# Kernel tuning notes

Hardware: AMD Instinct MI355X
Metric: run time of the kernel (lower is better)

The kernel has to match this reference:

```python
import jax, jax.numpy as jnp
import numpy as np

B, S, D = 4, 8192, 512


def setup_inputs() -> dict:
    key = jax.random.key(0)
    k1, k2, k3 = jax.random.split(key, 3)
    input_real = jax.random.normal(k1, (B, S, D), dtype=jnp.float32)
    input_imag = jax.random.normal(k2, (B, S, D), dtype=jnp.float32)
    weight = jax.random.uniform(k3, (B, S), dtype=jnp.float32)
    return {"input_real": input_real, "input_imag": input_imag, "weight": weight}


def reference(input_real, input_imag, weight):
    # Original: sum_s w[b,s] * (r_s r_s^T + i_s i_s^T)  and  sum_s w[b,s] * (i_s r_s^T - r_s i_s^T).
    # Algebraically equal to weighted Gram GEMMs X^T diag(w) Y; avoids the [B,S,D,D] intermediate.
    def wgram(x, y):
        # [B,S,D] x [B,S] x [B,S,D] -> [B,D,D]
        return jnp.einsum('bsd,bs,bse->bde', x, weight, y)

    output_r = wgram(input_real, input_real) + wgram(input_imag, input_imag)
    output_i = wgram(input_imag, input_real) - wgram(input_real, input_imag)
    return (output_r, output_i)
```

## Files before the change

### kernel.cpp

```cpp
#include <hip/hip_runtime.h>
#include <cstdint>
#include <cstddef>

#define NB 4
#define NS 8192
#define ND 512
#define NP 1024
#define BK 32

typedef __bf16 bf16x8 __attribute__((ext_vector_type(8)));
typedef float f32x4 __attribute__((ext_vector_type(4)));

union FragU { uint4 u; bf16x8 h; };

__device__ __forceinline__ unsigned short bf16rne(float x) {
  unsigned int u = __builtin_bit_cast(unsigned int, x);
  u += 0x7FFFu + ((u >> 16) & 1u);
  return (unsigned short)(u >> 16);
}

__device__ __forceinline__ void gload16(const void* g, void* l) {
  __builtin_amdgcn_global_load_lds(
      (const __attribute__((address_space(1))) unsigned int*)g,
      (__attribute__((address_space(3))) unsigned int*)l, 16, 0, 0);
}

__global__ __launch_bounds__(256)
void k_prep(const float* __restrict__ R, const float* __restrict__ I,
            const float* __restrict__ W, unsigned short* __restrict__ Yt) {
  __shared__ unsigned short L[64][66];
  const int t   = threadIdx.x;
  const int blk = blockIdx.x;
  const int sb  = blk & 127;
  const int pb  = (blk >> 7) & 15;
  const int b   = blk >> 11;
  const float* src = (pb < 8) ? R : I;
  const int col0 = (pb & 7) * 64;
  const int s0 = sb * 64;
  const int dl = (t & 15) * 4;
  const int sl0 = t >> 4;
#pragma unroll
  for (int r = 0; r < 4; ++r) {
    const int sl = sl0 + r * 16;
    const int s  = s0 + sl;
    const float sw = sqrtf(W[b * NS + s]);
    const float4 v = *(const float4*)(src + (size_t)(b * NS + s) * ND + col0 + dl);
    L[sl][dl + 0] = bf16rne(v.x * sw);
    L[sl][dl + 1] = bf16rne(v.y * sw);
    L[sl][dl + 2] = bf16rne(v.z * sw);
    L[sl][dl + 3] = bf16rne(v.w * sw);
  }
  __syncthreads();
  const int pl0 = t >> 3;
  const int sc  = (t & 7) * 8;
#pragma unroll
  for (int r = 0; r < 2; ++r) {
    const int pl = pl0 + r * 32;
    uint4 o;
    o.x = (unsigned)L[sc + 0][pl] | ((unsigned)L[sc + 1][pl] << 16);
    o.y = (unsigned)L[sc + 2][pl] | ((unsigned)L[sc + 3][pl] << 16);
    o.z = (unsigned)L[sc + 4][pl] | ((unsigned)L[sc + 5][pl] << 16);
    o.w = (unsigned)L[sc + 6][pl] | ((unsigned)L[sc + 7][pl] << 16);
    const int pg = pb * 64 + pl;
    *(uint4*)(Yt + (size_t)(b * NP + pg) * NS + (s0 + sc)) = o;
  }
}

__global__ __launch_bounds__(256, 2)
void k_gemm(const unsigned short* __restrict__ Yt, float* __restrict__ part,
            int ksteps) {
  __shared__ uint4 lds4[4096];
  char* lds = (char*)lds4;
  static const int TMp[10] = {0,1,1,2,2,2,3,3,3,3};
  static const int TNp[10] = {0,0,1,0,1,2,0,1,2,3};
  const int bid   = blockIdx.x;
  const int pos40 = bid % 40;
  const int split = bid / 40;
  const int b     = pos40 / 10;
  const int p     = pos40 % 10;
  const int tm = TMp[p], tn = TNp[p];
  const int t = threadIdx.x;
  const int l = t & 63;
  const int w = t >> 6;

  const int cj = l & 7;
  const int jj = l >> 3;
  const int ec = cj ^ jj;
  const int rbase = w * 16 + 2 * jj + (ec >> 2);
  const int colo  = (ec & 3) * 8;

  const int prow[4] = { tm * 128, 512 + tm * 128, tn * 128, 512 + tn * 128 };
  const unsigned short* gsrc[8];
  int dstoff[8];
#pragma unroll
  for (int tI = 0; tI < 4; ++tI)
#pragma unroll
    for (int i = 0; i < 2; ++i) {
      gsrc[tI * 2 + i] = Yt + (size_t)(b * NP + prow[tI] + i * 64 + rbase) * NS
                         + (size_t)split * ((size_t)ksteps * BK) + colo;
      dstoff[tI * 2 + i] = tI * 8192 + i * 4096 + w * 1024;
    }

  const int g  = l >> 4;
  const int e_ = l & 1;
  const int q  = (l >> 1) & 7;
  const int ibase = ((l & 15) >> 1) * 128 + ((64 * e_ + 16 * g) ^ (q << 4));

  const int wm = w & 1, wn = w >> 1;
  const int mfb = wm * 4096;
  const int nfb = wn * 4096;

  f32x4 accr[4][4], acci[4][4];
  const f32x4 zz = {0.f, 0.f, 0.f, 0.f};
#pragma unroll
  for (int a = 0; a < 4; ++a)
#pragma unroll
    for (int c = 0; c < 4; ++c) { accr[a][c] = zz; acci[a][c] = zz; }

#pragma unroll
  for (int u = 0; u < 8; ++u) { gload16(gsrc[u], lds + dstoff[u]); gsrc[u] += BK; }
  __syncthreads();

  int cur = 0;
  for (int ks = 0; ks < ksteps; ++ks) {
    const int cbase = cur * 32768;
    const int nbase = cbase ^ 32768;
    if (ks + 1 < ksteps) {
#pragma unroll
      for (int u = 0; u < 8; ++u) { gload16(gsrc[u], lds + nbase + dstoff[u]); gsrc[u] += BK; }
    }
    FragU ar[4], ai[4];
#pragma unroll
    for (int mf = 0; mf < 4; ++mf) {
      ar[mf].u = *(const uint4*)(lds + cbase +        mfb + mf * 1024 + ibase);
      ai[mf].u = *(const uint4*)(lds + cbase + 8192 + mfb + mf * 1024 + ibase);
    }
#pragma unroll
    for (int nf = 0; nf < 4; ++nf) {
      FragU br, bi, bin;
      br.u = *(const uint4*)(lds + cbase + 16384 + nfb + nf * 1024 + ibase);
      bi.u = *(const uint4*)(lds + cbase + 24576 + nfb + nf * 1024 + ibase);
      bin.u.x = bi.u.x ^ 0x80008000u;
      bin.u.y = bi.u.y ^ 0x80008000u;
      bin.u.z = bi.u.z ^ 0x80008000u;
      bin.u.w = bi.u.w ^ 0x80008000u;
#pragma unroll
      for (int mf = 0; mf < 4; ++mf) {
        accr[mf][nf] = __builtin_amdgcn_mfma_f32_16x16x32_bf16(ar[mf].h, br.h,  accr[mf][nf], 0, 0, 0);
        accr[mf][nf] = __builtin_amdgcn_mfma_f32_16x16x32_bf16(ai[mf].h, bi.h,  accr[mf][nf], 0, 0, 0);
        acci[mf][nf] = __builtin_amdgcn_mfma_f32_16x16x32_bf16(ai[mf].h, br.h,  acci[mf][nf], 0, 0, 0);
        acci[mf][nf] = __builtin_amdgcn_mfma_f32_16x16x32_bf16(ar[mf].h, bin.h, acci[mf][nf], 0, 0, 0);
      }
    }
    __syncthreads();
    cur ^= 1;
  }

  const size_t baser = ((size_t)(split * 40 + pos40) * 2 + 0) * 16384;
  const size_t basei = baser + 16384;
  const int lr = (l >> 4) * 4;
  const int lc = l & 15;
#pragma unroll
  for (int mf = 0; mf < 4; ++mf)
#pragma unroll
    for (int nf = 0; nf < 4; ++nf)
#pragma unroll
      for (int r = 0; r < 4; ++r) {
        const int mi = wm * 64 + mf * 16 + lr + r;
        const int ni = wn * 64 + nf * 16 + lc;
        part[baser + (size_t)mi * 128 + ni] = accr[mf][nf][r];
        part[basei + (size_t)mi * 128 + ni] = acci[mf][nf][r];
      }
}

__global__ __launch_bounds__(256)
void k_reduce(const float* __restrict__ part, float* __restrict__ out, int nsplit) {
  static const int TMp[10] = {0,1,1,2,2,2,3,3,3,3};
  static const int TNp[10] = {0,0,1,0,1,2,0,1,2,3};
  const int idx = blockIdx.x * 256 + threadIdx.x;
  const int ni = idx & 127;
  const int mi = (idx >> 7) & 127;
  const int o  = (idx >> 14) & 1;
  const int bp = idx >> 15;
  const int b = bp / 10, p = bp % 10;
  const size_t stride = (size_t)40 * 2 * 16384;
  size_t base = ((size_t)bp * 2 + o) * 16384 + (size_t)mi * 128 + ni;
  float a = 0.f;
  for (int s = 0; s < nsplit; ++s)
    a += part[base + (size_t)s * stride];
  const int d = TMp[p] * 128 + mi;
  const int e = TNp[p] * 128 + ni;
  out[(size_t)o * 1048576 + (size_t)b * 262144 + (size_t)d * 512 + e] = a;
}

__global__ __launch_bounds__(256)
void k_mirror(float* __restrict__ out) {
  __shared__ float T[64][65];
  static const int UM[6] = {0,0,0,1,1,2};
  static const int UN[6] = {1,2,3,2,3,3};
  const int m = blockIdx.x;
  const int sub = m & 3;
  const int b   = (m >> 2) & 3;
  const int o   = (m >> 4) & 1;
  const int u   = m >> 5;
  const int d0 = UM[u] * 128 + (sub & 1) * 64;
  const int e0 = UN[u] * 128 + ((sub >> 1) & 1) * 64;
  const float sign = o ? -1.f : 1.f;
  float* base = out + (size_t)o * 1048576 + (size_t)b * 262144;
  const int t  = threadIdx.x;
  const int c4 = (t & 15) * 4;
  const int r0 = t >> 4;
#pragma unroll
  for (int i = 0; i < 4; ++i) {
    const int r = r0 + i * 16;
    const float4 v = *(const float4*)(base + (size_t)(e0 + r) * 512 + d0 + c4);
    T[c4 + 0][r] = v.x; T[c4 + 1][r] = v.y;
    T[c4 + 2][r] = v.z; T[c4 + 3][r] = v.w;
  }
  __syncthreads();
#pragma unroll
  for (int i = 0; i < 4; ++i) {
    const int r = r0 + i * 16;
    float4 wv;
    wv.x = sign * T[r][c4 + 0]; wv.y = sign * T[r][c4 + 1];
    wv.z = sign * T[r][c4 + 2]; wv.w = sign * T[r][c4 + 3];
    *(float4*)(base + (size_t)(d0 + r) * 512 + e0 + c4) = wv;
  }
}

__global__ __launch_bounds__(256)
void k_fallback(const float* __restrict__ R, const float* __restrict__ I,
                const float* __restrict__ W, float* __restrict__ out) {
  __shared__ float Rd[64][32], Id[64][32], Re[64][32], Ie[64][32];
  const int blk = blockIdx.x;
  const int et = blk & 15, dt = (blk >> 4) & 15, b = blk >> 8;
  const int d0 = dt * 32, e0 = et * 32;
  const int t = threadIdx.x;
  const int dd = t >> 3;
  const int ee0 = (t & 7) * 4;
  float ar[4] = {0,0,0,0}, ai[4] = {0,0,0,0};
  for (int s0 = 0; s0 < NS; s0 += 64) {
#pragma unroll
    for (int k = 0; k < 8; ++k) {
      const int idx = t + k * 256;
      const int row = idx >> 5, col = idx & 31;
      const float sw = sqrtf(W[b * NS + s0 + row]);
      const size_t gr = (size_t)(b * NS + s0 + row) * ND;
      Rd[row][col] = R[gr + d0 + col] * sw;
      Id[row][col] = I[gr + d0 + col] * sw;
      Re[row][col] = R[gr + e0 + col] * sw;
      Ie[row][col] = I[gr + e0 + col] * sw;
    }
    __syncthreads();
    for (int s = 0; s < 64; ++s) {
      const float rd = Rd[s][dd], id = Id[s][dd];
#pragma unroll
      for (int j = 0; j < 4; ++j) {
        const float re = Re[s][ee0 + j], ie = Ie[s][ee0 + j];
        ar[j] += rd * re + id * ie;
        ai[j] += id * re - rd * ie;
      }
    }
    __syncthreads();
  }
  const size_t ob = (size_t)b * 262144;
#pragma unroll
  for (int j = 0; j < 4; ++j) {
    out[          ob + (size_t)(d0 + dd) * 512 + e0 + ee0 + j] = ar[j];
    out[1048576 + ob + (size_t)(d0 + dd) * 512 + e0 + ee0 + j] = ai[j];
  }
}

extern "C" void kernel_launch(void* const* d_in, const int* in_sizes, int n_in,
                              void* d_out, int out_size, void* d_ws, size_t ws_size,
                              hipStream_t stream) {
  const float* R = (const float*)d_in[0];
  const float* I = (const float*)d_in[1];
  const float* W = (const float*)d_in[2];
  float* out = (float*)d_out;
  const size_t ytBytes  = (size_t)NB * NP * NS * 2;
  const size_t perSplit = (size_t)40 * 2 * 16384 * 4;

  int SPLIT = 16;
  while (SPLIT > 2 && ytBytes + (size_t)SPLIT * perSplit > ws_size) SPLIT >>= 1;
  if (ytBytes + (size_t)SPLIT * perSplit > ws_size) {
    k_fallback<<<dim3(NB * 16 * 16), dim3(256), 0, stream>>>(R, I, W, out);
    return;
  }

  unsigned short* Yt = (unsigned short*)d_ws;
  float* part = (float*)((char*)d_ws + ytBytes);

  k_prep<<<dim3(NB * 16 * 128), dim3(256), 0, stream>>>(R, I, W, Yt);
  k_gemm<<<dim3(40 * SPLIT), dim3(256), 0, stream>>>(Yt, part, 256 / SPLIT);
  k_reduce<<<dim3(5120), dim3(256), 0, stream>>>(part, out, SPLIT);
  k_mirror<<<dim3(192), dim3(256), 0, stream>>>(out);
}
```

Baseline: 246.8 us.

## Balance GEMM work with stream-K style split across 512 blocks

Replaces the fixed split-K grid (40 tiles × SPLIT) with a stream-K style assignment. There are 40 tiles with 256 k-steps each, and each of 512 blocks takes a contiguous run of 20 k-steps, possibly spanning two tiles. Partial results go to per-block slots plus per-tile overflow slots, and the reduce kernel sums the contributing blocks per tile. It also swaps __syncthreads for explicit vmcnt waits and s_barrier, and raises wave priority during the MFMA section, to overlap loads with compute better. The intent is to fill the CUs evenly (512 = 2 blocks × 256 CUs) and cut pipeline-stall overhead. The cost is extra partial-buffer traffic and more complex reduction indexing.

```diff
diff --git a/kernel.cpp b/kernel.cpp
--- a/kernel.cpp
+++ b/kernel.cpp
@@ -67,127 +67,142 @@
 }
 
 __global__ __launch_bounds__(256, 2)
-void k_gemm(const unsigned short* __restrict__ Yt, float* __restrict__ part,
-            int ksteps) {
+void k_gemm(const unsigned short* __restrict__ Yt, float* __restrict__ part) {
   __shared__ uint4 lds4[4096];
   char* lds = (char*)lds4;
   static const int TMp[10] = {0,1,1,2,2,2,3,3,3,3};
   static const int TNp[10] = {0,0,1,0,1,2,0,1,2,3};
-  const int bid   = blockIdx.x;
-  const int pos40 = bid % 40;
-  const int split = bid / 40;
-  const int b     = pos40 / 10;
-  const int p     = pos40 % 10;
-  const int tm = TMp[p], tn = TNp[p];
+  const int j  = blockIdx.x;
+  const int g0 = j * 20;
+  const int g1 = g0 + 20;
+  const int p0 = g0 >> 8;
+  const int p1 = (g1 - 1) >> 8;
   const int t = threadIdx.x;
-  const int l = t & 63;
-  const int w = t >> 6;
-
-  const int cj = l & 7;
-  const int jj = l >> 3;
+  const int l = t & 63, w = t >> 6;
+
+  const int cj = l & 7, jj = l >> 3;
   const int ec = cj ^ jj;
   const int rbase = w * 16 + 2 * jj + (ec >> 2);
   const int colo  = (ec & 3) * 8;
-
-  const int prow[4] = { tm * 128, 512 + tm * 128, tn * 128, 512 + tn * 128 };
-  const unsigned short* gsrc[8];
   int dstoff[8];
 #pragma unroll
-  for (int tI = 0; tI < 4; ++tI)
-#pragma unroll
-    for (int i = 0; i < 2; ++i) {
-      gsrc[tI * 2 + i] = Yt + (size_t)(b * NP + prow[tI] + i * 64 + rbase) * NS
-                         + (size_t)split * ((size_t)ksteps * BK) + colo;
-      dstoff[tI * 2 + i] = tI * 8192 + i * 4096 + w * 1024;
+  for (int u = 0; u < 8; ++u) dstoff[u] = (u >> 1) * 8192 + (u & 1) * 4096 + w * 1024;
+
+  const int gfr = l >> 4, e_ = l & 1, q = (l >> 1) & 7;
+  const int ibase = ((l & 15) >> 1) * 128 + ((64 * e_ + 16 * gfr) ^ (q << 4));
+  const int wm = w & 1, wn = w >> 1;
+  const int mfb = wm * 4096, nfb = wn * 4096;
+  const int lr = (l >> 4) * 4, lc = l & 15;
+
+  for (int seg = 0; seg < 2; ++seg) {
+    int pos, k0, ns;
+    if (seg == 0) {
+      pos = p0; k0 = g0 & 255;
+      ns = 256 - k0; if (ns > 20) ns = 20;
+    } else {
+      if (p1 == p0) break;
+      pos = p1; k0 = 0; ns = g1 & 255;
     }
-
-  const int g  = l >> 4;
-  const int e_ = l & 1;
-  const int q  = (l >> 1) & 7;
-  const int ibase = ((l & 15) >> 1) * 128 + ((64 * e_ + 16 * g) ^ (q << 4));
-
-  const int wm = w & 1, wn = w >> 1;
-  const int mfb = wm * 4096;
-  const int nfb = wn * 4096;
-
-  f32x4 accr[4][4], acci[4][4];
-  const f32x4 zz = {0.f, 0.f, 0.f, 0.f};
-#pragma unroll
-  for (int a = 0; a < 4; ++a)
-#pragma unroll
-    for (int c = 0; c < 4; ++c) { accr[a][c] = zz; acci[a][c] = zz; }
-
-#pragma unroll
-  for (int u = 0; u < 8; ++u) { gload16(gsrc[u], lds + dstoff[u]); gsrc[u] += BK; }
-  __syncthreads();
-
-  int cur = 0;
-  for (int ks = 0; ks < ksteps; ++ks) {
-    const int cbase = cur * 32768;
-    const int nbase = cbase ^ 32768;
-    if (ks + 1 < ksteps) {
-#pragma unroll
-      for (int u = 0; u < 8; ++u) { gload16(gsrc[u], lds + nbase + dstoff[u]); gsrc[u] += BK; }
+    const int b = pos / 10, p = pos % 10;
+    const int tm = TMp[p], tn = TNp[p];
+    const int prow[4] = { tm * 128, 512 + tm * 128, tn * 128, 512 + tn * 128 };
+    const unsigned short* gsrc[8];
+#pragma unroll
+    for (int u = 0; u < 8; ++u)
+      gsrc[u] = Yt + (size_t)(b * NP + prow[u >> 1] + (u & 1) * 64 + rbase) * NS
+                + (size_t)k0 * BK + colo;
+
+    f32x4 accr[4][4], acci[4][4];
+    const f32x4 zz = {0.f, 0.f, 0.f, 0.f};
+#pragma unroll
+    for (int a = 0; a < 4; ++a)
+#pragma unroll
+      for (int c = 0; c < 4; ++c) { accr[a][c] = zz; acci[a][c] = zz; }
+
+#pragma unroll
+    for (int u = 0; u < 8; ++u) { gload16(gsrc[u], lds + dstoff[u]); gsrc[u] += BK; }
+    __builtin_amdgcn_sched_barrier(0);
+    asm volatile("s_waitcnt vmcnt(0)" ::: "memory");
+    __builtin_amdgcn_s_barrier();
+
+    int cur = 0;
+    for (int ks = 0; ks < ns; ++ks) {
+      const int cbase = cur * 32768;
+      if (ks + 1 < ns) {
+        const int nbase = cbase ^ 32768;
+#pragma unroll
+        for (int u = 0; u < 8; ++u) { gload16(gsrc[u], lds + nbase + dstoff[u]); gsrc[u] += BK; }
+        __builtin_amdgcn_sched_barrier(0);
+        asm volatile("s_waitcnt vmcnt(8)" ::: "memory");
+      } else {
+        asm volatile("s_waitcnt vmcnt(0)" ::: "memory");
+      }
+      __builtin_amdgcn_s_barrier();
+
+      FragU ar[4], ai[4];
+#pragma unroll
+      for (int mf = 0; mf < 4; ++mf) {
+        ar[mf].u = *(const uint4*)(lds + cbase +        mfb + mf * 1024 + ibase);
+        ai[mf].u = *(const uint4*)(lds + cbase + 8192 + mfb + mf * 1024 + ibase);
+      }
+      __builtin_amdgcn_s_setprio(1);
+#pragma unroll
+      for (int nf = 0; nf < 4; ++nf) {
+        FragU br, bi, bin;
+        br.u = *(const uint4*)(lds + cbase + 16384 + nfb + nf * 1024 + ibase);
+        bi.u = *(const uint4*)(lds + cbase + 24576 + nfb + nf * 1024 + ibase);
+        bin.u.x = bi.u.x ^ 0x80008000u;
+        bin.u.y = bi.u.y ^ 0x80008000u;
+        bin.u.z = bi.u.z ^ 0x80008000u;
+        bin.u.w = bi.u.w ^ 0x80008000u;
+#pragma unroll
+        for (int mf = 0; mf < 4; ++mf) {
+          accr[mf][nf] = __builtin_amdgcn_mfma_f32_16x16x32_bf16(ar[mf].h, br.h,  accr[mf][nf], 0, 0, 0);
+          accr[mf][nf] = __builtin_amdgcn_mfma_f32_16x16x32_bf16(ai[mf].h, bi.h,  accr[mf][nf], 0, 0, 0);
+          acci[mf][nf] = __builtin_amdgcn_mfma_f32_16x16x32_bf16(ai[mf].h, br.h,  acci[mf][nf], 0, 0, 0);
+          acci[mf][nf] = __builtin_amdgcn_mfma_f32_16x16x32_bf16(ar[mf].h, bin.h, acci[mf][nf], 0, 0, 0);
+        }
+      }
+      __builtin_amdgcn_s_setprio(0);
+      __builtin_amdgcn_s_barrier();
+      cur ^= 1;
     }
-    FragU ar[4], ai[4];
-#pragma unroll
-    for (int mf = 0; mf < 4; ++mf) {
-      ar[mf].u = *(const uint4*)(lds + cbase +        mfb + mf * 1024 + ibase);
-      ai[mf].u = *(const uint4*)(lds + cbase + 8192 + mfb + mf * 1024 + ibase);
-    }
-#pragma unroll
-    for (int nf = 0; nf < 4; ++nf) {
-      FragU br, bi, bin;
-      br.u = *(const uint4*)(lds + cbase + 16384 + nfb + nf * 1024 + ibase);
-      bi.u = *(const uint4*)(lds + cbase + 24576 + nfb + nf * 1024 + ibase);
-      bin.u.x = bi.u.x ^ 0x80008000u;
-      bin.u.y = bi.u.y ^ 0x80008000u;
-      bin.u.z = bi.u.z ^ 0x80008000u;
-      bin.u.w = bi.u.w ^ 0x80008000u;
-#pragma unroll
-      for (int mf = 0; mf < 4; ++mf) {
-        accr[mf][nf] = __builtin_amdgcn_mfma_f32_16x16x32_bf16(ar[mf].h, br.h,  accr[mf][nf], 0, 0, 0);
-        accr[mf][nf] = __builtin_amdgcn_mfma_f32_16x16x32_bf16(ai[mf].h, bi.h,  accr[mf][nf], 0, 0, 0);
-        acci[mf][nf] = __builtin_amdgcn_mfma_f32_16x16x32_bf16(ai[mf].h, br.h,  acci[mf][nf], 0, 0, 0);
-        acci[mf][nf] = __builtin_amdgcn_mfma_f32_16x16x32_bf16(ar[mf].h, bin.h, acci[mf][nf], 0, 0, 0);
-      }
-    }
-    __syncthreads();
-    cur ^= 1;
-  }
-
-  const size_t baser = ((size_t)(split * 40 + pos40) * 2 + 0) * 16384;
-  const size_t basei = baser + 16384;
-  const int lr = (l >> 4) * 4;
-  const int lc = l & 15;
-#pragma unroll
-  for (int mf = 0; mf < 4; ++mf)
-#pragma unroll
-    for (int nf = 0; nf < 4; ++nf)
-#pragma unroll
-      for (int r = 0; r < 4; ++r) {
-        const int mi = wm * 64 + mf * 16 + lr + r;
-        const int ni = wn * 64 + nf * 16 + lc;
-        part[baser + (size_t)mi * 128 + ni] = accr[mf][nf][r];
-        part[basei + (size_t)mi * 128 + ni] = acci[mf][nf][r];
-      }
+
+    const int slot = (seg == 0) ? j : (512 + pos);
+    const size_t baser = (size_t)slot * 32768;
+    const size_t basei = baser + 16384;
+#pragma unroll
+    for (int mf = 0; mf < 4; ++mf)
+#pragma unroll
+      for (int nf = 0; nf < 4; ++nf)
+#pragma unroll
+        for (int r = 0; r < 4; ++r) {
+          const int mi = wm * 64 + mf * 16 + lr + r;
+          const int ni = wn * 64 + nf * 16 + lc;
+          part[baser + (size_t)mi * 128 + ni] = accr[mf][nf][r];
+          part[basei + (size_t)mi * 128 + ni] = acci[mf][nf][r];
+        }
+  }
 }
 
 __global__ __launch_bounds__(256)
-void k_reduce(const float* __restrict__ part, float* __restrict__ out, int nsplit) {
+void k_reduce(const float* __restrict__ part, float* __restrict__ out) {
   static const int TMp[10] = {0,1,1,2,2,2,3,3,3,3};
   static const int TNp[10] = {0,0,1,0,1,2,0,1,2,3};
   const int idx = blockIdx.x * 256 + threadIdx.x;
   const int ni = idx & 127;
   const int mi = (idx >> 7) & 127;
   const int o  = (idx >> 14) & 1;
-  const int bp = idx >> 15;
-  const int b = bp / 10, p = bp % 10;
-  const size_t stride = (size_t)40 * 2 * 16384;
-  size_t base = ((size_t)bp * 2 + o) * 16384 + (size_t)mi * 128 + ni;
+  const int P  = idx >> 15;
+  const int jlo = (256 * P + 19) / 20;
+  const int jhi = (256 * P + 255) / 20;
+  const size_t off = (size_t)o * 16384 + (size_t)mi * 128 + ni;
   float a = 0.f;
-  for (int s = 0; s < nsplit; ++s)
-    a += part[base + (size_t)s * stride];
+  for (int s = jlo; s <= jhi; ++s)
+    a += part[(size_t)s * 32768 + off];
+  if ((256 * P) % 20)
+    a += part[(size_t)(512 + P) * 32768 + off];
+  const int b = P / 10, p = P % 10;
   const int d = TMp[p] * 128 + mi;
   const int e = TNp[p] * 128 + ni;
   out[(size_t)o * 1048576 + (size_t)b * 262144 + (size_t)d * 512 + e] = a;
@@ -255,19 +270,19 @@
     for (int s = 0; s < 64; ++s) {
       const float rd = Rd[s][dd], id = Id[s][dd];
 #pragma unroll
-      for (int j = 0; j < 4; ++j) {
-        const float re = Re[s][ee0 + j], ie = Ie[s][ee0 + j];
-        ar[j] += rd * re + id * ie;
-        ai[j] += id * re - rd * ie;
+      for (int jx = 0; jx < 4; ++jx) {
+        const float re = Re[s][ee0 + jx], ie = Ie[s][ee0 + jx];
+        ar[jx] += rd * re + id * ie;
+        ai[jx] += id * re - rd * ie;
       }
     }
     __syncthreads();
   }
   const size_t ob = (size_t)b * 262144;
 #pragma unroll
-  for (int j = 0; j < 4; ++j) {
-    out[          ob + (size_t)(d0 + dd) * 512 + e0 + ee0 + j] = ar[j];
-    out[1048576 + ob + (size_t)(d0 + dd) * 512 + e0 + ee0 + j] = ai[j];
+  for (int jx = 0; jx < 4; ++jx) {
+    out[          ob + (size_t)(d0 + dd) * 512 + e0 + ee0 + jx] = ar[jx];
+    out[1048576 + ob + (size_t)(d0 + dd) * 512 + e0 + ee0 + jx] = ai[jx];
   }
 }
 
@@ -278,12 +293,10 @@
   const float* I = (const float*)d_in[1];
   const float* W = (const float*)d_in[2];
   float* out = (float*)d_out;
-  const size_t ytBytes  = (size_t)NB * NP * NS * 2;
-  const size_t perSplit = (size_t)40 * 2 * 16384 * 4;
-
-  int SPLIT = 16;
-  while (SPLIT > 2 && ytBytes + (size_t)SPLIT * perSplit > ws_size) SPLIT >>= 1;
-  if (ytBytes + (size_t)SPLIT * perSplit > ws_size) {
+  const size_t ytBytes   = (size_t)NB * NP * NS * 2;
+  const size_t partBytes = (size_t)552 * 32768 * 4;
+
+  if (ws_size < ytBytes + partBytes) {
     k_fallback<<<dim3(NB * 16 * 16), dim3(256), 0, stream>>>(R, I, W, out);
     return;
   }
@@ -292,7 +305,7 @@
   float* part = (float*)((char*)d_ws + ytBytes);
 
   k_prep<<<dim3(NB * 16 * 128), dim3(256), 0, stream>>>(R, I, W, Yt);
-  k_gemm<<<dim3(40 * SPLIT), dim3(256), 0, stream>>>(Yt, part, 256 / SPLIT);
-  k_reduce<<<dim3(5120), dim3(256), 0, stream>>>(part, out, SPLIT);
+  k_gemm<<<dim3(512), dim3(256), 0, stream>>>(Yt, part);
+  k_reduce<<<dim3(5120), dim3(256), 0, stream>>>(part, out);
   k_mirror<<<dim3(192), dim3(256), 0, stream>>>(out);
 }
```

Result: faster. 234.3 us (-5.1%).
